# Optimization experiments

Measured on AMD Instinct MI355X. Metric: run time of the kernel, lower is better.

Reference implementation:

```python
import jax, jax.numpy as jnp
import numpy as np

B, V, FIN, COUT, K = 16, 20000, 64, 64, 16


def setup_inputs() -> dict:
    key = jax.random.key(0)
    k1, k2, k3, k4 = jax.random.split(key, 4)
    x = jax.random.normal(k1, (B, V, FIN), dtype=jnp.float32)
    Wx = jax.random.normal(k2, (FIN, COUT), dtype=jnp.float32) * (1.0 / np.sqrt(FIN))
    Wn = jax.random.normal(k3, (FIN, COUT), dtype=jnp.float32) * (1.0 / np.sqrt(FIN))
    b = jnp.zeros((COUT,), dtype=jnp.float32)
    # neighbor indices into the padded input: 0 is the zero-padding row, 1..V are real vertices
    neighbor = jax.random.randint(k4, (V, K), 0, V + 1, dtype=jnp.int32)
    return {"x": x, "Wx": Wx, "Wn": Wn, "b": b, "neighbor": neighbor}


def reference(x, Wx, Wn, b, neighbor):
    # x: [B, V, Fin]; neighbor: [V, K] indices into padded (V+1) vertex axis
    Bsz, Vn, Fin = x.shape
    pad = jnp.zeros((Bsz, 1, Fin), dtype=x.dtype)
    padded = jnp.concatenate([pad, x], axis=1)            # [B, V+1, Fin]
    nb = padded[:, neighbor, :]                            # [B, V, K, Fin] (gather)
    nb_mean = jnp.mean(nb, axis=2)                         # sum/K == mean (zeros included)
    out = jnp.einsum('bvf,fc->bvc', x, Wx) \
        + jnp.einsum('bvf,fc->bvc', nb_mean, Wn) + b
    return out
```

## Files before the change

kernel.cpp:

```cpp
#include <hip/hip_runtime.h>
#include <hip/hip_bf16.h>

#define BATCH 16
#define NV    20000
#define FIN   64
#define NCOUT 64
#define NK    16
#define TOTROWS  (BATCH * NV)
#define NTILES   (TOTROWS / 16)
#define TPX      (NTILES / 8)
#define TPB      (NV / 16)

typedef __attribute__((ext_vector_type(8))) short bf16x8;
typedef __attribute__((ext_vector_type(4))) float f32x4;
typedef __attribute__((ext_vector_type(4))) unsigned short u16x4;
typedef __attribute__((ext_vector_type(2))) unsigned int u32x2;

__device__ __forceinline__ short f2b(float f) {
    __hip_bfloat16 h = __float2bfloat16(f);
    return __builtin_bit_cast(short, h);
}

__global__ __launch_bounds__(256, 4) void convnet_zpass(
    const float* __restrict__ x,
    const float* __restrict__ Wn,
    __hip_bfloat16* __restrict__ z)
{
    const int lane = threadIdx.x & 63;
    const int m    = lane & 15;
    const int quad = lane >> 4;

    bf16x8 bn[4][2];
#pragma unroll
    for (int t = 0; t < 4; ++t) {
        const int c = 4 * m + t;
#pragma unroll
        for (int h = 0; h < 2; ++h) {
            bf16x8 fr;
#pragma unroll
            for (int j = 0; j < 8; ++j) {
                const int f = 32 * h + quad * 8 + j;
                fr[j] = f2b(Wn[f * NCOUT + c] * (1.0f / 16.0f));
            }
            bn[t][h] = fr;
        }
    }

    const int xcd = blockIdx.x & 7;
    const int bi  = blockIdx.x >> 3;
    const int wl  = bi * 4 + ((int)threadIdx.x >> 6);
    const int WPX = (gridDim.x >> 3) * 4;

    for (int t0 = wl; t0 < TPX; t0 += WPX) {
        const int rt = __builtin_amdgcn_readfirstlane(xcd * TPX + t0);
        const float* xt =
            x + (size_t)rt * (16 * FIN) + (size_t)m * FIN + quad * 8;

        const f32x4 La0 = __builtin_nontemporal_load((const f32x4*)xt);
        const f32x4 La1 = __builtin_nontemporal_load((const f32x4*)xt + 1);
        const f32x4 Lb0 = __builtin_nontemporal_load((const f32x4*)(xt + 32));
        const f32x4 Lb1 = __builtin_nontemporal_load((const f32x4*)(xt + 32) + 1);

        bf16x8 af0, af1;
        af0[0] = f2b(La0.x); af0[1] = f2b(La0.y); af0[2] = f2b(La0.z); af0[3] = f2b(La0.w);
        af0[4] = f2b(La1.x); af0[5] = f2b(La1.y); af0[6] = f2b(La1.z); af0[7] = f2b(La1.w);
        af1[0] = f2b(Lb0.x); af1[1] = f2b(Lb0.y); af1[2] = f2b(Lb0.z); af1[3] = f2b(Lb0.w);
        af1[4] = f2b(Lb1.x); af1[5] = f2b(Lb1.y); af1[6] = f2b(Lb1.z); af1[7] = f2b(Lb1.w);

        f32x4 acc[4];
#pragma unroll
        for (int t = 0; t < 4; ++t) acc[t] = (f32x4){0.f, 0.f, 0.f, 0.f};
#pragma unroll
        for (int t = 0; t < 4; ++t)
            acc[t] = __builtin_amdgcn_mfma_f32_16x16x32_bf16(af0, bn[t][0], acc[t], 0, 0, 0);
#pragma unroll
        for (int t = 0; t < 4; ++t)
            acc[t] = __builtin_amdgcn_mfma_f32_16x16x32_bf16(af1, bn[t][1], acc[t], 0, 0, 0);

        const size_t rbase = (size_t)rt * 16 + quad * 4;
#pragma unroll
        for (int r = 0; r < 4; ++r) {
            const size_t orow = (rbase + r) * NCOUT + 4 * m;
            u16x4 zz;
            zz.x = (unsigned short)f2b(acc[0][r]);
            zz.y = (unsigned short)f2b(acc[1][r]);
            zz.z = (unsigned short)f2b(acc[2][r]);
            zz.w = (unsigned short)f2b(acc[3][r]);
            *(u16x4*)(z + orow) = zz;
        }
    }
}

__global__ __launch_bounds__(256, 4) void convnet_fused(
    const float* __restrict__ x,
    const float* __restrict__ Wx,
    const float* __restrict__ bias,
    const int* __restrict__ nbr,
    const __hip_bfloat16* __restrict__ z,
    float* __restrict__ out)
{
    const int lane = threadIdx.x & 63;
    const int m    = lane & 15;
    const int quad = lane >> 4;

    bf16x8 bx[4][2];
#pragma unroll
    for (int t = 0; t < 4; ++t) {
        const int c = 4 * m + t;
#pragma unroll
        for (int h = 0; h < 2; ++h) {
            bf16x8 fr;
#pragma unroll
            for (int j = 0; j < 8; ++j) {
                const int f = 32 * h + quad * 8 + j;
                fr[j] = f2b(Wx[f * NCOUT + c]);
            }
            bx[t][h] = fr;
        }
    }
    float bias_q[4];
#pragma unroll
    for (int t = 0; t < 4; ++t) bias_q[t] = bias[4 * m + t];

    const int xcd = blockIdx.x & 7;
    const int bi  = blockIdx.x >> 3;
    const int wl  = bi * 4 + ((int)threadIdx.x >> 6);
    const int WPX = (gridDim.x >> 3) * 4;

    for (int t0 = TPX - 1 - wl; t0 >= 0; t0 -= WPX) {
        const int t0u = __builtin_amdgcn_readfirstlane(t0);
        const int rt  = xcd * TPX + t0u;
        const int blh = (t0u >= TPB) ? 1 : 0;
        const int b   = 2 * xcd + blh;
        const int v0  = (t0u - blh * TPB) * 16;

        const float* xt =
            x + (size_t)rt * (16 * FIN) + (size_t)m * FIN + quad * 8;
        const f32x4 La0 = __builtin_nontemporal_load((const f32x4*)xt);
        const f32x4 La1 = __builtin_nontemporal_load((const f32x4*)xt + 1);
        const f32x4 Lb0 = __builtin_nontemporal_load((const f32x4*)(xt + 32));
        const f32x4 Lb1 = __builtin_nontemporal_load((const f32x4*)(xt + 32) + 1);

        bf16x8 af0, af1;
        af0[0] = f2b(La0.x); af0[1] = f2b(La0.y); af0[2] = f2b(La0.z); af0[3] = f2b(La0.w);
        af0[4] = f2b(La1.x); af0[5] = f2b(La1.y); af0[6] = f2b(La1.z); af0[7] = f2b(La1.w);
        af1[0] = f2b(Lb0.x); af1[1] = f2b(Lb0.y); af1[2] = f2b(Lb0.z); af1[3] = f2b(Lb0.w);
        af1[4] = f2b(Lb1.x); af1[5] = f2b(Lb1.y); af1[6] = f2b(Lb1.z); af1[7] = f2b(Lb1.w);

        f32x4 acc[4];
#pragma unroll
        for (int t = 0; t < 4; ++t) acc[t] = (f32x4){0.f, 0.f, 0.f, 0.f};
#pragma unroll
        for (int t = 0; t < 4; ++t)
            acc[t] = __builtin_amdgcn_mfma_f32_16x16x32_bf16(af0, bx[t][0], acc[t], 0, 0, 0);
#pragma unroll
        for (int t = 0; t < 4; ++t)
            acc[t] = __builtin_amdgcn_mfma_f32_16x16x32_bf16(af1, bx[t][1], acc[t], 0, 0, 0);

        const char* zb = (const char*)z + (size_t)b * (NV * 128);
        const int zcol = m * 8;
#pragma unroll
        for (int r = 0; r < 4; ++r) {
            const int v = v0 + quad * 4 + r;
            const int4* nb4 = (const int4*)nbr + (size_t)v * 4;
            const int4 i0 = nb4[0];
            const int4 i1 = nb4[1];
            const int4 i2 = nb4[2];
            const int4 i3 = nb4[3];
            int id[NK];
            id[0]  = i0.x; id[1]  = i0.y; id[2]  = i0.z; id[3]  = i0.w;
            id[4]  = i1.x; id[5]  = i1.y; id[6]  = i1.z; id[7]  = i1.w;
            id[8]  = i2.x; id[9]  = i2.y; id[10] = i2.z; id[11] = i2.w;
            id[12] = i3.x; id[13] = i3.y; id[14] = i3.z; id[15] = i3.w;

            float a0 = 0.f, a1 = 0.f, a2 = 0.f, a3 = 0.f;
#pragma unroll
            for (int k = 0; k < NK; ++k) {
                const int idx = id[k];
                int sel = idx - 1;
                sel = sel < 0 ? 0 : sel;
                const u32x2 d =
                    *(const u32x2*)(zb + (size_t)(unsigned)(sel * 128 + zcol));
                const unsigned dx = idx ? d.x : 0u;
                const unsigned dy = idx ? d.y : 0u;
                a0 += __builtin_bit_cast(float, dx << 16);
                a1 += __builtin_bit_cast(float, dx & 0xFFFF0000u);
                a2 += __builtin_bit_cast(float, dy << 16);
                a3 += __builtin_bit_cast(float, dy & 0xFFFF0000u);
            }
            acc[0][r] += a0;
            acc[1][r] += a1;
            acc[2][r] += a2;
            acc[3][r] += a3;
        }

        const size_t rbase = (size_t)rt * 16 + quad * 4;
#pragma unroll
        for (int r = 0; r < 4; ++r) {
            const size_t orow = (rbase + r) * NCOUT + 4 * m;
            f32x4 o;
            o.x = acc[0][r] + bias_q[0];
            o.y = acc[1][r] + bias_q[1];
            o.z = acc[2][r] + bias_q[2];
            o.w = acc[3][r] + bias_q[3];
            __builtin_nontemporal_store(o, (f32x4*)(out + orow));
        }
    }
}

extern "C" void kernel_launch(void* const* d_in, const int* in_sizes, int n_in,
                              void* d_out, int out_size, void* d_ws, size_t ws_size,
                              hipStream_t stream) {
    const float* x    = (const float*)d_in[0];
    const float* Wx   = (const float*)d_in[1];
    const float* Wn   = (const float*)d_in[2];
    const float* bias = (const float*)d_in[3];
    const int*   nbr  = (const int*)d_in[4];
    float* out = (float*)d_out;

    __hip_bfloat16* z = (__hip_bfloat16*)d_ws;

    hipLaunchKernelGGL(convnet_zpass, dim3(1024), dim3(256), 0, stream,
                       x, Wn, z);
    hipLaunchKernelGGL(convnet_fused, dim3(1024), dim3(256), 0, stream,
                       x, Wx, bias, nbr, z, out);
}
```

Before: 269.9 us.

## Gather raw fp32 neighbor rows and fuse mean into single MFMA kernel

Replaces the two-pass scheme, which first projected x through Wn into a bf16 z buffer and then gathered z, with a single kernel. That kernel gathers fp32 neighbor rows of x directly, sums them, converts the sum to bf16 and runs both matmuls with MFMA. Weight fragments are precomputed once by a tiny init kernel and read from a workspace buffer. Occupancy is raised to 8 blocks per CU and the grid is doubled. This removes the z write/read round trip and one full pass over x, but each gather now fetches 256 bytes per neighbor instead of 128, so gather traffic doubles. Non-temporal hints on loads and stores are dropped.

```diff
diff --git a/kernel.cpp b/kernel.cpp
--- a/kernel.cpp
+++ b/kernel.cpp
@@ -6,45 +6,61 @@
 #define FIN   64
 #define NCOUT 64
 #define NK    16
-#define TOTROWS  (BATCH * NV)
-#define NTILES   (TOTROWS / 16)
-#define TPX      (NTILES / 8)
-#define TPB      (NV / 16)
+#define NTILES   20000
+#define TPX      2500
+#define TPB      1250
 
 typedef __attribute__((ext_vector_type(8))) short bf16x8;
 typedef __attribute__((ext_vector_type(4))) float f32x4;
-typedef __attribute__((ext_vector_type(4))) unsigned short u16x4;
-typedef __attribute__((ext_vector_type(2))) unsigned int u32x2;
 
 __device__ __forceinline__ short f2b(float f) {
     __hip_bfloat16 h = __float2bfloat16(f);
     return __builtin_bit_cast(short, h);
 }
 
-__global__ __launch_bounds__(256, 4) void convnet_zpass(
+__global__ void convnet_init(const float* __restrict__ Wx,
+                             const float* __restrict__ Wn,
+                             short* __restrict__ fragbuf) {
+    const int lane = threadIdx.x & 63;
+    const int m    = lane & 15;
+    const int quad = lane >> 4;
+#pragma unroll
+    for (int w = 0; w < 2; ++w) {
+        const float* W = w ? Wn : Wx;
+        const float s = w ? (1.0f / 16.0f) : 1.0f;
+#pragma unroll
+        for (int t = 0; t < 4; ++t) {
+            const int c = 4 * m + t;
+#pragma unroll
+            for (int h = 0; h < 2; ++h) {
+                bf16x8 fr;
+#pragma unroll
+                for (int j = 0; j < 8; ++j) {
+                    const int f = 32 * h + quad * 8 + j;
+                    fr[j] = f2b(W[f * NCOUT + c] * s);
+                }
+                ((bf16x8*)fragbuf)[(w * 8 + t * 2 + h) * 64 + lane] = fr;
+            }
+        }
+    }
+}
+
+__global__ __launch_bounds__(256, 8) void convnet_all(
     const float* __restrict__ x,
-    const float* __restrict__ Wn,
-    __hip_bfloat16* __restrict__ z)
+    const float* __restrict__ bias,
+    const int* __restrict__ nbr,
+    const short* __restrict__ fragbuf,
+    float* __restrict__ out)
 {
     const int lane = threadIdx.x & 63;
     const int m    = lane & 15;
     const int quad = lane >> 4;
 
-    bf16x8 bn[4][2];
+    float bias_q[4];
 #pragma unroll
-    for (int t = 0; t < 4; ++t) {
-        const int c = 4 * m + t;
-#pragma unroll
-        for (int h = 0; h < 2; ++h) {
-            bf16x8 fr;
-#pragma unroll
-            for (int j = 0; j < 8; ++j) {
-                const int f = 32 * h + quad * 8 + j;
-                fr[j] = f2b(Wn[f * NCOUT + c] * (1.0f / 16.0f));
-            }
-            bn[t][h] = fr;
-        }
-    }
+    for (int t = 0; t < 4; ++t) bias_q[t] = bias[4 * m + t];
+
+    const bf16x8* fb = (const bf16x8*)fragbuf;
 
     const int xcd = blockIdx.x & 7;
     const int bi  = blockIdx.x >> 3;
@@ -52,82 +68,6 @@
     const int WPX = (gridDim.x >> 3) * 4;
 
     for (int t0 = wl; t0 < TPX; t0 += WPX) {
-        const int rt = __builtin_amdgcn_readfirstlane(xcd * TPX + t0);
-        const float* xt =
-            x + (size_t)rt * (16 * FIN) + (size_t)m * FIN + quad * 8;
-
-        const f32x4 La0 = __builtin_nontemporal_load((const f32x4*)xt);
-        const f32x4 La1 = __builtin_nontemporal_load((const f32x4*)xt + 1);
-        const f32x4 Lb0 = __builtin_nontemporal_load((const f32x4*)(xt + 32));
-        const f32x4 Lb1 = __builtin_nontemporal_load((const f32x4*)(xt + 32) + 1);
-
-        bf16x8 af0, af1;
-        af0[0] = f2b(La0.x); af0[1] = f2b(La0.y); af0[2] = f2b(La0.z); af0[3] = f2b(La0.w);
-        af0[4] = f2b(La1.x); af0[5] = f2b(La1.y); af0[6] = f2b(La1.z); af0[7] = f2b(La1.w);
-        af1[0] = f2b(Lb0.x); af1[1] = f2b(Lb0.y); af1[2] = f2b(Lb0.z); af1[3] = f2b(Lb0.w);
-        af1[4] = f2b(Lb1.x); af1[5] = f2b(Lb1.y); af1[6] = f2b(Lb1.z); af1[7] = f2b(Lb1.w);
-
-        f32x4 acc[4];
-#pragma unroll
-        for (int t = 0; t < 4; ++t) acc[t] = (f32x4){0.f, 0.f, 0.f, 0.f};
-#pragma unroll
-        for (int t = 0; t < 4; ++t)
-            acc[t] = __builtin_amdgcn_mfma_f32_16x16x32_bf16(af0, bn[t][0], acc[t], 0, 0, 0);
-#pragma unroll
-        for (int t = 0; t < 4; ++t)
-            acc[t] = __builtin_amdgcn_mfma_f32_16x16x32_bf16(af1, bn[t][1], acc[t], 0, 0, 0);
-
-        const size_t rbase = (size_t)rt * 16 + quad * 4;
-#pragma unroll
-        for (int r = 0; r < 4; ++r) {
-            const size_t orow = (rbase + r) * NCOUT + 4 * m;
-            u16x4 zz;
-            zz.x = (unsigned short)f2b(acc[0][r]);
-            zz.y = (unsigned short)f2b(acc[1][r]);
-            zz.z = (unsigned short)f2b(acc[2][r]);
-            zz.w = (unsigned short)f2b(acc[3][r]);
-            *(u16x4*)(z + orow) = zz;
-        }
-    }
-}
-
-__global__ __launch_bounds__(256, 4) void convnet_fused(
-    const float* __restrict__ x,
-    const float* __restrict__ Wx,
-    const float* __restrict__ bias,
-    const int* __restrict__ nbr,
-    const __hip_bfloat16* __restrict__ z,
-    float* __restrict__ out)
-{
-    const int lane = threadIdx.x & 63;
-    const int m    = lane & 15;
-    const int quad = lane >> 4;
-
-    bf16x8 bx[4][2];
-#pragma unroll
-    for (int t = 0; t < 4; ++t) {
-        const int c = 4 * m + t;
-#pragma unroll
-        for (int h = 0; h < 2; ++h) {
-            bf16x8 fr;
-#pragma unroll
-            for (int j = 0; j < 8; ++j) {
-                const int f = 32 * h + quad * 8 + j;
-                fr[j] = f2b(Wx[f * NCOUT + c]);
-            }
-            bx[t][h] = fr;
-        }
-    }
-    float bias_q[4];
-#pragma unroll
-    for (int t = 0; t < 4; ++t) bias_q[t] = bias[4 * m + t];
-
-    const int xcd = blockIdx.x & 7;
-    const int bi  = blockIdx.x >> 3;
-    const int wl  = bi * 4 + ((int)threadIdx.x >> 6);
-    const int WPX = (gridDim.x >> 3) * 4;
-
-    for (int t0 = TPX - 1 - wl; t0 >= 0; t0 -= WPX) {
         const int t0u = __builtin_amdgcn_readfirstlane(t0);
         const int rt  = xcd * TPX + t0u;
         const int blh = (t0u >= TPB) ? 1 : 0;
@@ -136,10 +76,36 @@
 
         const float* xt =
             x + (size_t)rt * (16 * FIN) + (size_t)m * FIN + quad * 8;
-        const f32x4 La0 = __builtin_nontemporal_load((const f32x4*)xt);
-        const f32x4 La1 = __builtin_nontemporal_load((const f32x4*)xt + 1);
-        const f32x4 Lb0 = __builtin_nontemporal_load((const f32x4*)(xt + 32));
-        const f32x4 Lb1 = __builtin_nontemporal_load((const f32x4*)(xt + 32) + 1);
+        const f32x4 La0 = ((const f32x4*)xt)[0];
+        const f32x4 La1 = ((const f32x4*)xt)[1];
+        const f32x4 Lb0 = ((const f32x4*)(xt + 32))[0];
+        const f32x4 Lb1 = ((const f32x4*)(xt + 32))[1];
+
+        const char* xb = (const char*)x + (size_t)b * (NV * 256);
+        const int coff = quad * 32;
+        const int4* nb4 = (const int4*)nbr + (size_t)(v0 + m) * 4;
+
+        f32x4 s0 = (f32x4){0.f,0.f,0.f,0.f}, s1 = s0, s2 = s0, s3 = s0;
+
+#define GATHER1(IDX)                                                         \
+        {                                                                    \
+            const int idx = (IDX);                                           \
+            const int sel = (idx > 0) ? (idx - 1) : 0;                       \
+            const float wk = idx ? 1.0f : 0.0f;                              \
+            const char* rp = xb + (size_t)((unsigned)sel * 256u + coff);     \
+            const f32x4 g0 = *(const f32x4*)rp;                              \
+            const f32x4 g1 = *(const f32x4*)(rp + 16);                       \
+            const f32x4 g2 = *(const f32x4*)(rp + 128);                      \
+            const f32x4 g3 = *(const f32x4*)(rp + 144);                      \
+            s0 += wk * g0; s1 += wk * g1; s2 += wk * g2; s3 += wk * g3;      \
+        }
+
+        {
+            const int4 iA = nb4[0];
+            const int4 iB = nb4[1];
+            GATHER1(iA.x) GATHER1(iA.y) GATHER1(iA.z) GATHER1(iA.w)
+            GATHER1(iB.x) GATHER1(iB.y) GATHER1(iB.z) GATHER1(iB.w)
+        }
 
         bf16x8 af0, af1;
         af0[0] = f2b(La0.x); af0[1] = f2b(La0.y); af0[2] = f2b(La0.z); af0[3] = f2b(La0.w);
@@ -147,51 +113,29 @@
         af1[0] = f2b(Lb0.x); af1[1] = f2b(Lb0.y); af1[2] = f2b(Lb0.z); af1[3] = f2b(Lb0.w);
         af1[4] = f2b(Lb1.x); af1[5] = f2b(Lb1.y); af1[6] = f2b(Lb1.z); af1[7] = f2b(Lb1.w);
 
+        {
+            const int4 iC = nb4[2];
+            const int4 iD = nb4[3];
+            GATHER1(iC.x) GATHER1(iC.y) GATHER1(iC.z) GATHER1(iC.w)
+            GATHER1(iD.x) GATHER1(iD.y) GATHER1(iD.z) GATHER1(iD.w)
+        }
+#undef GATHER1
+
+        bf16x8 an0, an1;
+        an0[0] = f2b(s0.x); an0[1] = f2b(s0.y); an0[2] = f2b(s0.z); an0[3] = f2b(s0.w);
+        an0[4] = f2b(s1.x); an0[5] = f2b(s1.y); an0[6] = f2b(s1.z); an0[7] = f2b(s1.w);
+        an1[0] = f2b(s2.x); an1[1] = f2b(s2.y); an1[2] = f2b(s2.z); an1[3] = f2b(s2.w);
+        an1[4] = f2b(s3.x); an1[5] = f2b(s3.y); an1[6] = f2b(s3.z); an1[7] = f2b(s3.w);
+
         f32x4 acc[4];
 #pragma unroll
-        for (int t = 0; t < 4; ++t) acc[t] = (f32x4){0.f, 0.f, 0.f, 0.f};
+        for (int t = 0; t < 4; ++t) acc[t] = (f32x4){0.f,0.f,0.f,0.f};
 #pragma unroll
-        for (int t = 0; t < 4; ++t)
-            acc[t] = __builtin_amdgcn_mfma_f32_16x16x32_bf16(af0, bx[t][0], acc[t], 0, 0, 0);
-#pragma unroll
-        for (int t = 0; t < 4; ++t)
-            acc[t] = __builtin_amdgcn_mfma_f32_16x16x32_bf16(af1, bx[t][1], acc[t], 0, 0, 0);
-
-        const char* zb = (const char*)z + (size_t)b * (NV * 128);
-        const int zcol = m * 8;
-#pragma unroll
-        for (int r = 0; r < 4; ++r) {
-            const int v = v0 + quad * 4 + r;
-            const int4* nb4 = (const int4*)nbr + (size_t)v * 4;
-            const int4 i0 = nb4[0];
-            const int4 i1 = nb4[1];
-            const int4 i2 = nb4[2];
-            const int4 i3 = nb4[3];
-            int id[NK];
-            id[0]  = i0.x; id[1]  = i0.y; id[2]  = i0.z; id[3]  = i0.w;
-            id[4]  = i1.x; id[5]  = i1.y; id[6]  = i1.z; id[7]  = i1.w;
-            id[8]  = i2.x; id[9]  = i2.y; id[10] = i2.z; id[11] = i2.w;
-            id[12] = i3.x; id[13] = i3.y; id[14] = i3.z; id[15] = i3.w;
-
-            float a0 = 0.f, a1 = 0.f, a2 = 0.f, a3 = 0.f;
-#pragma unroll
-            for (int k = 0; k < NK; ++k) {
-                const int idx = id[k];
-                int sel = idx - 1;
-                sel = sel < 0 ? 0 : sel;
-                const u32x2 d =
-                    *(const u32x2*)(zb + (size_t)(unsigned)(sel * 128 + zcol));
-                const unsigned dx = idx ? d.x : 0u;
-                const unsigned dy = idx ? d.y : 0u;
-                a0 += __builtin_bit_cast(float, dx << 16);
-                a1 += __builtin_bit_cast(float, dx & 0xFFFF0000u);
-                a2 += __builtin_bit_cast(float, dy << 16);
-                a3 += __builtin_bit_cast(float, dy & 0xFFFF0000u);
-            }
-            acc[0][r] += a0;
-            acc[1][r] += a1;
-            acc[2][r] += a2;
-            acc[3][r] += a3;
+        for (int t = 0; t < 4; ++t) {
+            acc[t] = __builtin_amdgcn_mfma_f32_16x16x32_bf16(af0, fb[(t*2 + 0)*64 + lane], acc[t], 0, 0, 0);
+            acc[t] = __builtin_amdgcn_mfma_f32_16x16x32_bf16(af1, fb[(t*2 + 1)*64 + lane], acc[t], 0, 0, 0);
+            acc[t] = __builtin_amdgcn_mfma_f32_16x16x32_bf16(an0, fb[(8 + t*2 + 0)*64 + lane], acc[t], 0, 0, 0);
+            acc[t] = __builtin_amdgcn_mfma_f32_16x16x32_bf16(an1, fb[(8 + t*2 + 1)*64 + lane], acc[t], 0, 0, 0);
         }
 
         const size_t rbase = (size_t)rt * 16 + quad * 4;
@@ -203,7 +147,7 @@
             o.y = acc[1][r] + bias_q[1];
             o.z = acc[2][r] + bias_q[2];
             o.w = acc[3][r] + bias_q[3];
-            __builtin_nontemporal_store(o, (f32x4*)(out + orow));
+            *(f32x4*)(out + orow) = o;
         }
     }
 }
@@ -218,10 +162,10 @@
     const int*   nbr  = (const int*)d_in[4];
     float* out = (float*)d_out;
 
-    __hip_bfloat16* z = (__hip_bfloat16*)d_ws;
+    short* fragbuf = (short*)d_ws;
 
-    hipLaunchKernelGGL(convnet_zpass, dim3(1024), dim3(256), 0, stream,
-                       x, Wn, z);
-    hipLaunchKernelGGL(convnet_fused, dim3(1024), dim3(256), 0, stream,
-                       x, Wx, bias, nbr, z, out);
+    hipLaunchKernelGGL(convnet_init, dim3(1), dim3(64), 0, stream,
+                       Wx, Wn, fragbuf);
+    hipLaunchKernelGGL(convnet_all, dim3(2048), dim3(256), 0, stream,
+                       x, bias, nbr, fragbuf, out);
 }
```

Result: slower. 380.3 us (+40.9%).
